# Kernel tuning notes

Measured on AMD Instinct MI355X. Metric: run time of the kernel, lower is better.

## Reference

```python
import jax, jax.numpy as jnp
import numpy as np

B, S, D, H, DH, DF, L = 8, 785, 128, 8, 64, 512, 6
HW = 28
CIN = 512


def setup_inputs() -> dict:
    key = jax.random.key(0)
    ks = iter(jax.random.split(key, 40))
    n = lambda shape, s=0.02: jax.random.normal(next(ks), shape, dtype=jnp.float32) * s
    inp = {}
    # conv stem (1x1 conv, no bias) + BN (eval mode) params
    inp["conv_w"] = n((D, CIN), 0.05)
    inp["bn_gamma"] = 1.0 + n((D,), 0.05)
    inp["bn_beta"] = n((D,), 0.05)
    inp["bn_mean"] = n((D,), 0.05)
    inp["bn_var"] = 1.0 + 0.1 * jax.random.uniform(next(ks), (D,), dtype=jnp.float32)
    # encoder embeddings
    inp["pos_emb"] = n((1, S, D))
    inp["cls_token"] = n((1, 1, D))
    # per-layer stacked params
    inp["Wq"] = n((L, D, H * DH)); inp["bq"] = jnp.zeros((L, H * DH), jnp.float32)
    inp["Wk"] = n((L, D, H * DH)); inp["bk"] = jnp.zeros((L, H * DH), jnp.float32)
    inp["Wv"] = n((L, D, H * DH)); inp["bv"] = jnp.zeros((L, H * DH), jnp.float32)
    inp["Wo"] = n((L, H * DH, D)); inp["bo"] = jnp.zeros((L, D), jnp.float32)
    inp["ln1_g"] = jnp.ones((L, D), jnp.float32); inp["ln1_b"] = jnp.zeros((L, D), jnp.float32)
    inp["ffn_w1"] = n((L, D, DF)); inp["ffn_b1"] = jnp.zeros((L, DF), jnp.float32)
    inp["ffn_w2"] = n((L, DF, D)); inp["ffn_b2"] = jnp.zeros((L, D), jnp.float32)
    inp["ln2_g"] = jnp.ones((L, D), jnp.float32); inp["ln2_b"] = jnp.zeros((L, D), jnp.float32)
    # MLP head (both Linear layers bias=False)
    inp["proj_w1"] = n((D, 512)); inp["proj_w2"] = n((512, 1))
    # forward tensor args
    inp["enc_inputs"] = jnp.ones((B, S), dtype=jnp.int32)  # no padding -> mask all False
    inp["x"] = jax.random.normal(next(ks), (B, CIN, HW, HW), dtype=jnp.float32)
    inp["y"] = jax.random.normal(next(ks), (B, CIN, HW, HW), dtype=jnp.float32)
    return inp


def _layer_norm(z, g, b, eps=1e-12):
    mu = z.mean(-1, keepdims=True)
    var = ((z - mu) ** 2).mean(-1, keepdims=True)
    return (z - mu) * jax.lax.rsqrt(var + eps) * g + b


def reference(conv_w, bn_gamma, bn_beta, bn_mean, bn_var, pos_emb, cls_token,
              Wq, bq, Wk, bk, Wv, bv, Wo, bo, ln1_g, ln1_b,
              ffn_w1, ffn_b1, ffn_w2, ffn_b2, ln2_g, ln2_b,
              proj_w1, proj_w2, enc_inputs, x, y):
    def conv_enc(z):
        z = jnp.einsum('bchw,dc->bdhw', z, conv_w)  # 1x1 conv, no bias
        inv = jax.lax.rsqrt(bn_var + 1e-5)
        z = (z - bn_mean[None, :, None, None]) * inv[None, :, None, None]
        z = z * bn_gamma[None, :, None, None] + bn_beta[None, :, None, None]
        return jax.nn.relu(z)

    x = conv_enc(x)
    y = conv_enc(y)
    max_val = jnp.maximum(x.max(), y.max())
    x = x / max_val
    y = y / max_val
    b = x.shape[0]
    x = x.reshape(b, D, -1).transpose(0, 2, 1)  # [b, hw, D]
    y = y.reshape(b, D, -1).transpose(0, 2, 1)

    cls = jnp.broadcast_to(cls_token, (b, 1, D))
    xs = jnp.concatenate([cls, x], axis=1) + pos_emb    # evolving stream (K, V)
    xf = jnp.concatenate([cls, y], axis=1) + pos_emb    # fixed stream (Q)

    pad_mask = (enc_inputs == 0)[:, None, None, :]      # [b,1,1,S], broadcast over heads & queries
    scale = 1.0 / jnp.sqrt(jnp.float32(DH))

    for i in range(L):
        q = (xf @ Wq[i] + bq[i]).reshape(b, S, H, DH).transpose(0, 2, 1, 3)
        k = (xs @ Wk[i] + bk[i]).reshape(b, S, H, DH).transpose(0, 2, 1, 3)
        v = (xs @ Wv[i] + bv[i]).reshape(b, S, H, DH).transpose(0, 2, 1, 3)
        scores = jnp.einsum('bhqd,bhkd->bhqk', q, k) * scale
        scores = jnp.where(pad_mask, jnp.float32(-1e9), scores)
        probs = jax.nn.softmax(scores, axis=-1)
        ctx = jnp.einsum('bhqk,bhkd->bhqd', probs, v)
        ctx = ctx.transpose(0, 2, 1, 3).reshape(b, S, H * DH)
        att = ctx @ Wo[i] + bo[i]
        xs = _layer_norm(xs + att, ln1_g[i], ln1_b[i])
        ff = jax.nn.gelu(xs @ ffn_w1[i] + ffn_b1[i], approximate=False) @ ffn_w2[i] + ffn_b2[i]
        xs = _layer_norm(ff + xs, ln2_g[i], ln2_b[i])

    h = jax.nn.relu(xs[:, 0, :] @ proj_w1)
    return h @ proj_w2  # [b, 1]
```

## Files before the change

kernel.cpp:

```cpp
#include <hip/hip_runtime.h>
#include <hip/hip_bf16.h>
#include <math.h>

typedef float f4 __attribute__((ext_vector_type(4)));
typedef _Float16 h8 __attribute__((ext_vector_type(8)));
typedef float f32x4 __attribute__((ext_vector_type(4)));

#define NB 8
#define NS 785
#define ND 128
#define NH 8
#define NDH 64
#define NDF 512
#define NL 6
#define NP 784
#define NCIN 512
#define NM (NB*NS)

__global__ __launch_bounds__(256) void conv_bn_relu_kernel(
    const float* __restrict__ x, const float* __restrict__ w,
    const float* __restrict__ gamma, const float* __restrict__ beta,
    const float* __restrict__ mean, const float* __restrict__ var,
    float* __restrict__ enc, unsigned int* __restrict__ maxv)
{
    __shared__ float xt[64][17];
    __shared__ float wt[64][132];
    __shared__ float red[4];
    const int b  = blockIdx.y;
    const int p0 = blockIdx.x * 16;
    const int t  = threadIdx.x;
    const int pl = (t & 3) * 4;
    const int dl = (t >> 2) * 2;
    float acc[2][4] = {};
    for (int c0 = 0; c0 < NCIN; c0 += 64) {
        __syncthreads();
        {
            int cc = t >> 2, pp = (t & 3) * 4;
            f4 v = *(const f4*)&x[(size_t)(b*NCIN + c0 + cc)*NP + p0 + pp];
            xt[cc][pp+0] = v[0]; xt[cc][pp+1] = v[1]; xt[cc][pp+2] = v[2]; xt[cc][pp+3] = v[3];
        }
        #pragma unroll
        for (int i = 0; i < 8; i++) {
            int e = t + i*256;
            int d = e >> 4, c4 = (e & 15) * 4;
            f4 v = *(const f4*)&w[(size_t)d*NCIN + c0 + c4];
            wt[c4+0][d] = v[0]; wt[c4+1][d] = v[1]; wt[c4+2][d] = v[2]; wt[c4+3][d] = v[3];
        }
        __syncthreads();
        #pragma unroll 8
        for (int cc = 0; cc < 64; cc++) {
            float w0 = wt[cc][dl], w1 = wt[cc][dl+1];
            float x0 = xt[cc][pl+0], x1 = xt[cc][pl+1], x2 = xt[cc][pl+2], x3 = xt[cc][pl+3];
            acc[0][0] += w0*x0; acc[0][1] += w0*x1; acc[0][2] += w0*x2; acc[0][3] += w0*x3;
            acc[1][0] += w1*x0; acc[1][1] += w1*x1; acc[1][2] += w1*x2; acc[1][3] += w1*x3;
        }
    }
    float lmax = 0.f;
    #pragma unroll
    for (int i = 0; i < 2; i++) {
        int d = dl + i;
        float inv = rsqrtf(var[d] + 1e-5f);
        float sc = gamma[d] * inv;
        float sh = beta[d] - mean[d] * sc;
        #pragma unroll
        for (int j = 0; j < 4; j++) {
            float vo = fmaxf(acc[i][j]*sc + sh, 0.f);
            lmax = fmaxf(lmax, vo);
            enc[(size_t)(b*NP + p0 + pl + j)*ND + d] = vo;
        }
    }
    for (int o = 1; o < 64; o <<= 1) lmax = fmaxf(lmax, __shfl_xor(lmax, o));
    if ((t & 63) == 0) red[t >> 6] = lmax;
    __syncthreads();
    if (t == 0) {
        float m2 = fmaxf(fmaxf(red[0], red[1]), fmaxf(red[2], red[3]));
        atomicMax(maxv, __float_as_uint(m2));
    }
}

__global__ void assemble_kernel(
    const float* __restrict__ encx, const float* __restrict__ ency,
    const float* __restrict__ cls, const float* __restrict__ pos,
    const float* __restrict__ maxv, float* __restrict__ xs, float* __restrict__ xf)
{
    int i = blockIdx.x*256 + threadIdx.x;
    int d = i & 127;
    int s = (i >> 7) % NS;
    int b = i / (NS*ND);
    float inv = 1.f / maxv[0];
    float pv = pos[s*ND + d];
    float xv, yv;
    if (s == 0) { xv = cls[d]; yv = cls[d]; }
    else {
        int idx = (b*NP + s - 1)*ND + d;
        xv = encx[idx]*inv; yv = ency[idx]*inv;
    }
    xs[i] = xv + pv;
    xf[i] = yv + pv;
}

template<int ACT, int OUTH>
__global__ __launch_bounds__(256) void mfma_gemm_kernel(
    const float* __restrict__ A, const float* __restrict__ W,
    const float* __restrict__ bias, void* __restrict__ Cv,
    int M, int N, int K)
{
    __shared__ _Float16 At[128][40];
    __shared__ _Float16 Wt[64][40];
    const int bm = blockIdx.x * 128, bn = blockIdx.y * 64;
    const int t = threadIdx.x;
    const int lane = t & 63;
    const int wave = t >> 6;
    const int m0 = (wave >> 1) * 64;
    const int n0 = (wave & 1) * 32;
    const int lrow = lane & 15, lhi = lane >> 4;
    f32x4 acc[4][2] = {};

    for (int k0 = 0; k0 < K; k0 += 32) {
        __syncthreads();
        {
            int r = t >> 1, sg = (t & 1) * 16;
            int row = bm + r;
            h8 lo = {}, hi = {};
            if (row < M) {
                const float* src = &A[(size_t)row*K + k0 + sg];
                f4 v0 = *(const f4*)&src[0];
                f4 v1 = *(const f4*)&src[4];
                f4 v2 = *(const f4*)&src[8];
                f4 v3 = *(const f4*)&src[12];
                lo = h8{(_Float16)v0[0],(_Float16)v0[1],(_Float16)v0[2],(_Float16)v0[3],
                        (_Float16)v1[0],(_Float16)v1[1],(_Float16)v1[2],(_Float16)v1[3]};
                hi = h8{(_Float16)v2[0],(_Float16)v2[1],(_Float16)v2[2],(_Float16)v2[3],
                        (_Float16)v3[0],(_Float16)v3[1],(_Float16)v3[2],(_Float16)v3[3]};
            }
            *(h8*)&At[r][sg]     = lo;
            *(h8*)&At[r][sg + 8] = hi;
        }
        {
            int kk = t >> 3, nseg = (t & 7) * 8;
            const float* src = &W[(size_t)(k0 + kk)*N + bn + nseg];
            #pragma unroll
            for (int i = 0; i < 8; i++) Wt[nseg + i][kk] = (_Float16)src[i];
        }
        __syncthreads();
        h8 af[4], bf[2];
        #pragma unroll
        for (int mf = 0; mf < 4; mf++) af[mf] = *(const h8*)&At[m0 + mf*16 + lrow][lhi*8];
        #pragma unroll
        for (int nf = 0; nf < 2; nf++) bf[nf] = *(const h8*)&Wt[n0 + nf*16 + lrow][lhi*8];
        #pragma unroll
        for (int mf = 0; mf < 4; mf++)
            #pragma unroll
            for (int nf = 0; nf < 2; nf++)
                acc[mf][nf] = __builtin_amdgcn_mfma_f32_16x16x32_f16(af[mf], bf[nf], acc[mf][nf], 0, 0, 0);
    }

    #pragma unroll
    for (int nf = 0; nf < 2; nf++) {
        int col = bn + n0 + nf*16 + lrow;
        float bv = bias[col];
        #pragma unroll
        for (int mf = 0; mf < 4; mf++) {
            #pragma unroll
            for (int r = 0; r < 4; r++) {
                int row = bm + m0 + mf*16 + lhi*4 + r;
                if (row < M) {
                    float v = acc[mf][nf][r] + bv;
                    if (ACT == 1) v = 0.5f * v * (1.f + erff(v * 0.70710678118654752f));
                    if (OUTH) ((_Float16*)Cv)[(size_t)row*N + col] = (_Float16)v;
                    else      ((float*)Cv)[(size_t)row*N + col] = v;
                }
            }
        }
    }
}

__global__ __launch_bounds__(256) void attn_mfma_kernel(
    const _Float16* __restrict__ Q, const _Float16* __restrict__ K,
    const _Float16* __restrict__ V, const int* __restrict__ enc,
    float* __restrict__ O)
{
    __shared__ _Float16 Ks[64][68];
    __shared__ _Float16 Vt[64][68];
    __shared__ _Float16 Ps[4][16][68];
    const int b = blockIdx.x, h = blockIdx.y, qt = blockIdx.z;
    const int q0 = qt * 64;
    const int t = threadIdx.x, lane = t & 63, w = t >> 6;
    const int lrow = lane & 15, lhi = lane >> 4;

    h8 qf[2] = {};
    {
        int qrow = q0 + w*16 + lrow;
        if (qrow < NS) {
            const _Float16* src = &Q[(size_t)(b*NS + qrow)*512 + h*64];
            #pragma unroll
            for (int ks = 0; ks < 2; ks++)
                qf[ks] = *(const h8*)&src[ks*32 + lhi*8];
        }
    }

    float m[4], l[4];
    f32x4 acc[4] = {};
    #pragma unroll
    for (int r = 0; r < 4; r++) { m[r] = -INFINITY; l[r] = 0.f; }

    for (int kt = 0; kt < 13; kt++) {
        int k0 = kt * 64;
        __syncthreads();
        {
            int r = t >> 2, c0 = (t & 3) * 16;
            int s = k0 + r;
            h8 lo = {}, hi = {};
            if (s < NS) {
                const _Float16* src = &K[(size_t)(b*NS + s)*512 + h*64 + c0];
                lo = *(const h8*)&src[0];
                hi = *(const h8*)&src[8];
            }
            *(h8*)&Ks[r][c0]     = lo;
            *(h8*)&Ks[r][c0 + 8] = hi;
        }
        {
            int r = t >> 2, c0 = (t & 3) * 16;
            int s = k0 + r;
            h8 a = {}, c = {};
            if (s < NS) {
                const _Float16* src = &V[(size_t)(b*NS + s)*512 + h*64 + c0];
                a = *(const h8*)&src[0];
                c = *(const h8*)&src[8];
            }
            #pragma unroll
            for (int i = 0; i < 8; i++) Vt[c0 + i][r] = a[i];
            #pragma unroll
            for (int i = 0; i < 8; i++) Vt[c0 + 8 + i][r] = c[i];
        }
        __syncthreads();

        f32x4 sc[4] = {};
        #pragma unroll
        for (int nf = 0; nf < 4; nf++)
            #pragma unroll
            for (int ks = 0; ks < 2; ks++) {
                h8 bf = *(const h8*)&Ks[nf*16 + lrow][ks*32 + lhi*8];
                sc[nf] = __builtin_amdgcn_mfma_f32_16x16x32_f16(qf[ks], bf, sc[nf], 0, 0, 0);
            }
        #pragma unroll
        for (int nf = 0; nf < 4; nf++) {
            int kk = k0 + nf*16 + lrow;
            bool oob = (kk >= NS);
            float madd = (!oob && enc[b*NS + kk] == 0) ? -1e9f : 0.f;
            #pragma unroll
            for (int r = 0; r < 4; r++) {
                float v = sc[nf][r] * 0.125f + madd;
                sc[nf][r] = oob ? -INFINITY : v;
            }
        }
        float corr[4];
        #pragma unroll
        for (int r = 0; r < 4; r++) {
            float mt = fmaxf(fmaxf(sc[0][r], sc[1][r]), fmaxf(sc[2][r], sc[3][r]));
            mt = fmaxf(mt, __shfl_xor(mt, 1));
            mt = fmaxf(mt, __shfl_xor(mt, 2));
            mt = fmaxf(mt, __shfl_xor(mt, 4));
            mt = fmaxf(mt, __shfl_xor(mt, 8));
            float mn = fmaxf(m[r], mt);
            corr[r] = __expf(m[r] - mn);
            m[r] = mn;
            float ps = 0.f;
            #pragma unroll
            for (int nf = 0; nf < 4; nf++) {
                float p = __expf(sc[nf][r] - mn);
                sc[nf][r] = p;
                ps += p;
            }
            ps += __shfl_xor(ps, 1);
            ps += __shfl_xor(ps, 2);
            ps += __shfl_xor(ps, 4);
            ps += __shfl_xor(ps, 8);
            l[r] = l[r] * corr[r] + ps;
        }
        #pragma unroll
        for (int nf = 0; nf < 4; nf++)
            #pragma unroll
            for (int r = 0; r < 4; r++)
                Ps[w][lhi*4 + r][nf*16 + lrow] = (_Float16)sc[nf][r];
        asm volatile("s_waitcnt lgkmcnt(0)" ::: "memory");
        __builtin_amdgcn_sched_barrier(0);
        #pragma unroll
        for (int nf = 0; nf < 4; nf++)
            #pragma unroll
            for (int r = 0; r < 4; r++) acc[nf][r] *= corr[r];
        #pragma unroll
        for (int nf = 0; nf < 4; nf++)
            #pragma unroll
            for (int ks = 0; ks < 2; ks++) {
                h8 pf = *(const h8*)&Ps[w][lrow][ks*32 + lhi*8];
                h8 vf = *(const h8*)&Vt[nf*16 + lrow][ks*32 + lhi*8];
                acc[nf] = __builtin_amdgcn_mfma_f32_16x16x32_f16(pf, vf, acc[nf], 0, 0, 0);
            }
    }
    #pragma unroll
    for (int nf = 0; nf < 4; nf++)
        #pragma unroll
        for (int r = 0; r < 4; r++) {
            int row = q0 + w*16 + lhi*4 + r;
            if (row < NS)
                O[(size_t)(b*NS + row)*512 + h*64 + nf*16 + lrow] = acc[nf][r] / l[r];
        }
}

__global__ __launch_bounds__(256) void res_ln_kernel(
    const float* X, const float* __restrict__ R,
    const float* __restrict__ g, const float* __restrict__ be, float* out)
{
    int row = blockIdx.x*4 + (threadIdx.x >> 6);
    int lane = threadIdx.x & 63;
    const float* xr = X + (size_t)row*128;
    const float* rr = R + (size_t)row*128;
    float a0 = xr[lane] + rr[lane];
    float a1 = xr[lane+64] + rr[lane+64];
    float s = a0 + a1;
    for (int o = 1; o < 64; o <<= 1) s += __shfl_xor(s, o);
    float mean = s * (1.f/128.f);
    float e0 = a0 - mean, e1 = a1 - mean;
    float vs = e0*e0 + e1*e1;
    for (int o = 1; o < 64; o <<= 1) vs += __shfl_xor(vs, o);
    float rstd = rsqrtf(vs * (1.f/128.f) + 1e-12f);
    out[(size_t)row*128 + lane]      = e0*rstd*g[lane] + be[lane];
    out[(size_t)row*128 + lane + 64] = e1*rstd*g[lane+64] + be[lane+64];
}

__global__ __launch_bounds__(512) void head_kernel(
    const float* __restrict__ xs, const float* __restrict__ w1,
    const float* __restrict__ w2, float* __restrict__ out)
{
    __shared__ float red[8];
    int b = blockIdx.x, j = threadIdx.x;
    const float* xr = xs + (size_t)(b*NS)*128;
    float acc = 0.f;
    #pragma unroll 8
    for (int c = 0; c < 128; c++) acc += xr[c] * w1[c*512 + j];
    acc = fmaxf(acc, 0.f);
    float sv = acc * w2[j];
    for (int o = 1; o < 64; o <<= 1) sv += __shfl_xor(sv, o);
    if ((j & 63) == 0) red[j >> 6] = sv;
    __syncthreads();
    if (j == 0) {
        float r = 0.f;
        #pragma unroll
        for (int i = 0; i < 8; i++) r += red[i];
        out[b] = r;
    }
}

extern "C" void kernel_launch(void* const* d_in, const int* in_sizes, int n_in,
                              void* d_out, int out_size, void* d_ws, size_t ws_size,
                              hipStream_t stream)
{
    const float* conv_w   = (const float*)d_in[0];
    const float* bn_gamma = (const float*)d_in[1];
    const float* bn_beta  = (const float*)d_in[2];
    const float* bn_mean  = (const float*)d_in[3];
    const float* bn_var   = (const float*)d_in[4];
    const float* pos_emb  = (const float*)d_in[5];
    const float* cls_tok  = (const float*)d_in[6];
    const float* Wq = (const float*)d_in[7];  const float* bq = (const float*)d_in[8];
    const float* Wk = (const float*)d_in[9];  const float* bk = (const float*)d_in[10];
    const float* Wv = (const float*)d_in[11]; const float* bv = (const float*)d_in[12];
    const float* Wo = (const float*)d_in[13]; const float* bo = (const float*)d_in[14];
    const float* ln1_g = (const float*)d_in[15]; const float* ln1_b = (const float*)d_in[16];
    const float* fw1 = (const float*)d_in[17]; const float* fb1 = (const float*)d_in[18];
    const float* fw2 = (const float*)d_in[19]; const float* fb2 = (const float*)d_in[20];
    const float* ln2_g = (const float*)d_in[21]; const float* ln2_b = (const float*)d_in[22];
    const float* pw1 = (const float*)d_in[23]; const float* pw2 = (const float*)d_in[24];
    const int*   enc = (const int*)d_in[25];
    const float* x   = (const float*)d_in[26];
    const float* y   = (const float*)d_in[27];
    float* out = (float*)d_out;

    float* ws   = (float*)d_ws;
    float* maxv = ws;
    float* xs   = ws + 64;
    float* xf   = xs + 803840;
    float* ctx  = xf + 803840;
    float* fmid = ctx + 3215360;
    float* fout = fmid + 3215360;
    float* encx = fout + 803840;
    float* ency = encx + 802816;
    _Float16* qh = (_Float16*)(ency + 802816);
    _Float16* kh = qh + 3215360;
    _Float16* vh = kh + 3215360;

    hipMemsetAsync(d_ws, 0, 256, stream);

    dim3 cgrid(49, NB);
    conv_bn_relu_kernel<<<cgrid, 256, 0, stream>>>(x, conv_w, bn_gamma, bn_beta,
        bn_mean, bn_var, encx, (unsigned int*)maxv);
    conv_bn_relu_kernel<<<cgrid, 256, 0, stream>>>(y, conv_w, bn_gamma, bn_beta,
        bn_mean, bn_var, ency, (unsigned int*)maxv);

    assemble_kernel<<<3140, 256, 0, stream>>>(encx, ency, cls_tok, pos_emb, maxv, xs, xf);

    for (int i = 0; i < NL; i++) {
        const size_t wofs = (size_t)i * 128 * 512;
        mfma_gemm_kernel<0,1><<<dim3(50,8), 256, 0, stream>>>(xf, Wq + wofs, bq + i*512, qh, NM, 512, 128);
        mfma_gemm_kernel<0,1><<<dim3(50,8), 256, 0, stream>>>(xs, Wk + wofs, bk + i*512, kh, NM, 512, 128);
        mfma_gemm_kernel<0,1><<<dim3(50,8), 256, 0, stream>>>(xs, Wv + wofs, bv + i*512, vh, NM, 512, 128);
        attn_mfma_kernel<<<dim3(8,8,13), 256, 0, stream>>>(qh, kh, vh, enc, ctx);
        mfma_gemm_kernel<0,0><<<dim3(50,2), 256, 0, stream>>>(ctx, Wo + wofs, bo + i*128, fout, NM, 128, 512);
        res_ln_kernel<<<1570, 256, 0, stream>>>(xs, fout, ln1_g + i*128, ln1_b + i*128, xs);
        mfma_gemm_kernel<1,0><<<dim3(50,8), 256, 0, stream>>>(xs, fw1 + wofs, fb1 + i*512, fmid, NM, 512, 128);
        mfma_gemm_kernel<0,0><<<dim3(50,2), 256, 0, stream>>>(fmid, fw2 + wofs, fb2 + i*128, fout, NM, 128, 512);
        res_ln_kernel<<<1570, 256, 0, stream>>>(xs, fout, ln2_g + i*128, ln2_b + i*128, xs);
    }

    head_kernel<<<8, 512, 0, stream>>>(xs, pw1, pw2, out);
}
```

Measured before the change: 1.213 ms.

## Store GEMM operands and intermediates in fp16 and pre-convert weights once

Weights are converted to fp16 once per call in a new conversion kernel, and the activations feeding the GEMMs (xs/xf copies, attention context, FFN hidden) are now written as fp16 by their producer kernels. The GEMM kernels load fp16 directly instead of reading fp32 and converting, which halves global memory traffic for A and W operands and removes per-tile conversion work. The costs are an extra kernel launch, extra fp16 shadow writes in res_ln and assemble, and somewhat lower precision for the stored intermediates.

```diff
diff --git a/kernel.cpp b/kernel.cpp
--- a/kernel.cpp
+++ b/kernel.cpp
@@ -78,10 +78,32 @@
     }
 }
 
+__global__ __launch_bounds__(256) void wconv_kernel(
+    const float* __restrict__ w0, const float* __restrict__ w1,
+    const float* __restrict__ w2, const float* __restrict__ w3,
+    const float* __restrict__ w4, const float* __restrict__ w5,
+    _Float16* o0, _Float16* o1, _Float16* o2,
+    _Float16* o3, _Float16* o4, _Float16* o5)
+{
+    int t = blockIdx.x*256 + threadIdx.x;
+    int type = t / 393216, off = t % 393216;
+    const float* in; _Float16* outp;
+    switch (type) {
+        case 0: in = w0; outp = o0; break;
+        case 1: in = w1; outp = o1; break;
+        case 2: in = w2; outp = o2; break;
+        case 3: in = w3; outp = o3; break;
+        case 4: in = w4; outp = o4; break;
+        default: in = w5; outp = o5; break;
+    }
+    outp[off] = (_Float16)in[off];
+}
+
 __global__ void assemble_kernel(
     const float* __restrict__ encx, const float* __restrict__ ency,
     const float* __restrict__ cls, const float* __restrict__ pos,
-    const float* __restrict__ maxv, float* __restrict__ xs, float* __restrict__ xf)
+    const float* __restrict__ maxv, float* __restrict__ xs,
+    _Float16* __restrict__ xsh, _Float16* __restrict__ xfh)
 {
     int i = blockIdx.x*256 + threadIdx.x;
     int d = i & 127;
@@ -95,13 +117,15 @@
         int idx = (b*NP + s - 1)*ND + d;
         xv = encx[idx]*inv; yv = ency[idx]*inv;
     }
-    xs[i] = xv + pv;
-    xf[i] = yv + pv;
+    float sx = xv + pv, fx = yv + pv;
+    xs[i]  = sx;
+    xsh[i] = (_Float16)sx;
+    xfh[i] = (_Float16)fx;
 }
 
 template<int ACT, int OUTH>
 __global__ __launch_bounds__(256) void mfma_gemm_kernel(
-    const float* __restrict__ A, const float* __restrict__ W,
+    const _Float16* __restrict__ A, const _Float16* __restrict__ W,
     const float* __restrict__ bias, void* __restrict__ Cv,
     int M, int N, int K)
 {
@@ -123,24 +147,18 @@
             int row = bm + r;
             h8 lo = {}, hi = {};
             if (row < M) {
-                const float* src = &A[(size_t)row*K + k0 + sg];
-                f4 v0 = *(const f4*)&src[0];
-                f4 v1 = *(const f4*)&src[4];
-                f4 v2 = *(const f4*)&src[8];
-                f4 v3 = *(const f4*)&src[12];
-                lo = h8{(_Float16)v0[0],(_Float16)v0[1],(_Float16)v0[2],(_Float16)v0[3],
-                        (_Float16)v1[0],(_Float16)v1[1],(_Float16)v1[2],(_Float16)v1[3]};
-                hi = h8{(_Float16)v2[0],(_Float16)v2[1],(_Float16)v2[2],(_Float16)v2[3],
-                        (_Float16)v3[0],(_Float16)v3[1],(_Float16)v3[2],(_Float16)v3[3]};
+                const _Float16* src = &A[(size_t)row*K + k0 + sg];
+                lo = *(const h8*)&src[0];
+                hi = *(const h8*)&src[8];
             }
             *(h8*)&At[r][sg]     = lo;
             *(h8*)&At[r][sg + 8] = hi;
         }
         {
             int kk = t >> 3, nseg = (t & 7) * 8;
-            const float* src = &W[(size_t)(k0 + kk)*N + bn + nseg];
-            #pragma unroll
-            for (int i = 0; i < 8; i++) Wt[nseg + i][kk] = (_Float16)src[i];
+            h8 v = *(const h8*)&W[(size_t)(k0 + kk)*N + bn + nseg];
+            #pragma unroll
+            for (int i = 0; i < 8; i++) Wt[nseg + i][kk] = v[i];
         }
         __syncthreads();
         h8 af[4], bf[2];
@@ -178,7 +196,7 @@
 __global__ __launch_bounds__(256) void attn_mfma_kernel(
     const _Float16* __restrict__ Q, const _Float16* __restrict__ K,
     const _Float16* __restrict__ V, const int* __restrict__ enc,
-    float* __restrict__ O)
+    _Float16* __restrict__ O)
 {
     __shared__ _Float16 Ks[64][68];
     __shared__ _Float16 Vt[64][68];
@@ -304,13 +322,14 @@
         for (int r = 0; r < 4; r++) {
             int row = q0 + w*16 + lhi*4 + r;
             if (row < NS)
-                O[(size_t)(b*NS + row)*512 + h*64 + nf*16 + lrow] = acc[nf][r] / l[r];
+                O[(size_t)(b*NS + row)*512 + h*64 + nf*16 + lrow] = (_Float16)(acc[nf][r] / l[r]);
         }
 }
 
 __global__ __launch_bounds__(256) void res_ln_kernel(
     const float* X, const float* __restrict__ R,
-    const float* __restrict__ g, const float* __restrict__ be, float* out)
+    const float* __restrict__ g, const float* __restrict__ be,
+    float* out, _Float16* __restrict__ outh)
 {
     int row = blockIdx.x*4 + (threadIdx.x >> 6);
     int lane = threadIdx.x & 63;
@@ -325,8 +344,12 @@
     float vs = e0*e0 + e1*e1;
     for (int o = 1; o < 64; o <<= 1) vs += __shfl_xor(vs, o);
     float rstd = rsqrtf(vs * (1.f/128.f) + 1e-12f);
-    out[(size_t)row*128 + lane]      = e0*rstd*g[lane] + be[lane];
-    out[(size_t)row*128 + lane + 64] = e1*rstd*g[lane+64] + be[lane+64];
+    float o0 = e0*rstd*g[lane] + be[lane];
+    float o1 = e1*rstd*g[lane+64] + be[lane+64];
+    out[(size_t)row*128 + lane]       = o0;
+    out[(size_t)row*128 + lane + 64]  = o1;
+    outh[(size_t)row*128 + lane]      = (_Float16)o0;
+    outh[(size_t)row*128 + lane + 64] = (_Float16)o1;
 }
 
 __global__ __launch_bounds__(512) void head_kernel(
@@ -377,20 +400,32 @@
     const float* y   = (const float*)d_in[27];
     float* out = (float*)d_out;
 
-    float* ws   = (float*)d_ws;
-    float* maxv = ws;
-    float* xs   = ws + 64;
-    float* xf   = xs + 803840;
-    float* ctx  = xf + 803840;
-    float* fmid = ctx + 3215360;
-    float* fout = fmid + 3215360;
-    float* encx = fout + 803840;
-    float* ency = encx + 802816;
-    _Float16* qh = (_Float16*)(ency + 802816);
-    _Float16* kh = qh + 3215360;
-    _Float16* vh = kh + 3215360;
+    char* base = (char*)d_ws;
+    size_t o = 0;
+    auto alloc = [&](size_t bytes) { void* p = base + o; o += bytes; return p; };
+    float* maxv     = (float*)alloc(256);
+    float* xs       = (float*)alloc(3215360);
+    float* fout     = (float*)alloc(3215360);
+    float* encx     = (float*)alloc(3211264);
+    float* ency     = (float*)alloc(3211264);
+    _Float16* xsh   = (_Float16*)alloc(1607680);
+    _Float16* xfh   = (_Float16*)alloc(1607680);
+    _Float16* qh    = (_Float16*)alloc(6430720);
+    _Float16* kh    = (_Float16*)alloc(6430720);
+    _Float16* vh    = (_Float16*)alloc(6430720);
+    _Float16* ctxh  = (_Float16*)alloc(6430720);
+    _Float16* fmidh = (_Float16*)alloc(6430720);
+    _Float16* wqh   = (_Float16*)alloc(786432);
+    _Float16* wkh   = (_Float16*)alloc(786432);
+    _Float16* wvh   = (_Float16*)alloc(786432);
+    _Float16* woh   = (_Float16*)alloc(786432);
+    _Float16* f1h   = (_Float16*)alloc(786432);
+    _Float16* f2h   = (_Float16*)alloc(786432);
 
     hipMemsetAsync(d_ws, 0, 256, stream);
+
+    wconv_kernel<<<9216, 256, 0, stream>>>(Wq, Wk, Wv, Wo, fw1, fw2,
+                                           wqh, wkh, wvh, woh, f1h, f2h);
 
     dim3 cgrid(49, NB);
     conv_bn_relu_kernel<<<cgrid, 256, 0, stream>>>(x, conv_w, bn_gamma, bn_beta,
@@ -398,19 +433,20 @@
     conv_bn_relu_kernel<<<cgrid, 256, 0, stream>>>(y, conv_w, bn_gamma, bn_beta,
         bn_mean, bn_var, ency, (unsigned int*)maxv);
 
-    assemble_kernel<<<3140, 256, 0, stream>>>(encx, ency, cls_tok, pos_emb, maxv, xs, xf);
+    assemble_kernel<<<3140, 256, 0, stream>>>(encx, ency, cls_tok, pos_emb, maxv,
+                                              xs, xsh, xfh);
 
     for (int i = 0; i < NL; i++) {
         const size_t wofs = (size_t)i * 128 * 512;
-        mfma_gemm_kernel<0,1><<<dim3(50,8), 256, 0, stream>>>(xf, Wq + wofs, bq + i*512, qh, NM, 512, 128);
-        mfma_gemm_kernel<0,1><<<dim3(50,8), 256, 0, stream>>>(xs, Wk + wofs, bk + i*512, kh, NM, 512, 128);
-        mfma_gemm_kernel<0,1><<<dim3(50,8), 256, 0, stream>>>(xs, Wv + wofs, bv + i*512, vh, NM, 512, 128);
-        attn_mfma_kernel<<<dim3(8,8,13), 256, 0, stream>>>(qh, kh, vh, enc, ctx);
-        mfma_gemm_kernel<0,0><<<dim3(50,2), 256, 0, stream>>>(ctx, Wo + wofs, bo + i*128, fout, NM, 128, 512);
-        res_ln_kernel<<<1570, 256, 0, stream>>>(xs, fout, ln1_g + i*128, ln1_b + i*128, xs);
-        mfma_gemm_kernel<1,0><<<dim3(50,8), 256, 0, stream>>>(xs, fw1 + wofs, fb1 + i*512, fmid, NM, 512, 128);
-        mfma_gemm_kernel<0,0><<<dim3(50,2), 256, 0, stream>>>(fmid, fw2 + wofs, fb2 + i*128, fout, NM, 128, 512);
-        res_ln_kernel<<<1570, 256, 0, stream>>>(xs, fout, ln2_g + i*128, ln2_b + i*128, xs);
+        mfma_gemm_kernel<0,1><<<dim3(50,8), 256, 0, stream>>>(xfh, wqh + wofs, bq + i*512, qh, NM, 512, 128);
+        mfma_gemm_kernel<0,1><<<dim3(50,8), 256, 0, stream>>>(xsh, wkh + wofs, bk + i*512, kh, NM, 512, 128);
+        mfma_gemm_kernel<0,1><<<dim3(50,8), 256, 0, stream>>>(xsh, wvh + wofs, bv + i*512, vh, NM, 512, 128);
+        attn_mfma_kernel<<<dim3(8,8,13), 256, 0, stream>>>(qh, kh, vh, enc, ctxh);
+        mfma_gemm_kernel<0,0><<<dim3(50,2), 256, 0, stream>>>(ctxh, woh + wofs, bo + i*128, fout, NM, 128, 512);
+        res_ln_kernel<<<1570, 256, 0, stream>>>(xs, fout, ln1_g + i*128, ln1_b + i*128, xs, xsh);
+        mfma_gemm_kernel<1,1><<<dim3(50,8), 256, 0, stream>>>(xsh, f1h + wofs, fb1 + i*512, fmidh, NM, 512, 128);
+        mfma_gemm_kernel<0,0><<<dim3(50,2), 256, 0, stream>>>(fmidh, f2h + wofs, fb2 + i*128, fout, NM, 128, 512);
+        res_ln_kernel<<<1570, 256, 0, stream>>>(xs, fout, ln2_g + i*128, ln2_b + i*128, xs, xsh);
     }
 
     head_kernel<<<8, 512, 0, stream>>>(xs, pw1, pw2, out);
```

Result: faster. 1.130 ms (-6.8%).
